# Optimization experiments

Hardware: AMD Instinct MI355X
Metric: run time of the kernel (lower is better)

## Reference

```python
import jax, jax.numpy as jnp
import numpy as np

N = 50000      # nodes per graph type
E = 600000     # directed edges
F = 64         # raw node feature length
H = 128        # hidden / embedding size (embedding == h, so no padding needed)
STEPS = 4
G = 64         # graphs in batch


def setup_inputs() -> dict:
    key = jax.random.key(0)
    ks = jax.random.split(key, 16)
    s = 1.0 / np.sqrt(H)
    inp = {
        "atom_x": jax.random.normal(ks[0], (N, F), jnp.float32),
        "voro_x": jax.random.normal(ks[1], (N, F), jnp.float32),
        "atom_edge_index": jax.random.randint(ks[2], (2, E), 0, N, jnp.int64),
        "voro_edge_index": jax.random.randint(ks[3], (2, E), 0, N, jnp.int64),
        "batch": jnp.sort(jax.random.randint(ks[4], (N,), 0, G, jnp.int64)),
        # input embeddings (bias=False)
        "W_atom_in": jax.random.normal(ks[5], (F, H), jnp.float32) / np.sqrt(F),
        "W_voro_in": jax.random.normal(ks[6], (F, H), jnp.float32) / np.sqrt(F),
        # GatedGraphConv per-step message weights [STEPS, H, H]
        "atom_W": jax.random.normal(ks[7], (STEPS, H, H), jnp.float32) * s,
        "voro_W": jax.random.normal(ks[8], (STEPS, H, H), jnp.float32) * s,
        # GRUCell params (torch layout: W_ih [3H, H], gates ordered r, z, n)
        "atom_Wih": jax.random.normal(ks[9], (3 * H, H), jnp.float32) * s,
        "atom_Whh": jax.random.normal(ks[10], (3 * H, H), jnp.float32) * s,
        "atom_bih": jnp.zeros((3 * H,), jnp.float32),
        "atom_bhh": jnp.zeros((3 * H,), jnp.float32),
        "voro_Wih": jax.random.normal(ks[11], (3 * H, H), jnp.float32) * s,
        "voro_Whh": jax.random.normal(ks[12], (3 * H, H), jnp.float32) * s,
        "voro_bih": jnp.zeros((3 * H,), jnp.float32),
        "voro_bhh": jnp.zeros((3 * H,), jnp.float32),
        # prediction head Linear(2H, 1)
        "pred_W": jax.random.normal(ks[13], (2 * H, 1), jnp.float32) * s,
        "pred_b": jnp.zeros((1,), jnp.float32),
    }
    return inp


def _gated_graph_conv(x, edge_index, W, Wih, Whh, bih, bhh):
    """PyG GatedGraphConv with aggr='add': per step, m = h @ W_l, scatter-add
    messages from source to target, then GRUCell(m, h)."""
    src, dst = edge_index[0], edge_index[1]

    def step(h, Wl):
        m = h @ Wl                                           # [N, H]
        agg = jax.ops.segment_sum(m[src], dst, num_segments=N)  # gather+scatter-add
        gi = agg @ Wih.T + bih                               # input gates
        gh = h @ Whh.T + bhh                                 # hidden gates
        ir, iz, inn = jnp.split(gi, 3, axis=-1)
        hr, hz, hn = jnp.split(gh, 3, axis=-1)
        r = jax.nn.sigmoid(ir + hr)
        z = jax.nn.sigmoid(iz + hz)
        n = jnp.tanh(inn + r * hn)
        h_new = (1.0 - z) * n + z * h
        return h_new, None

    h, _ = jax.lax.scan(step, x, W)
    return h


def _mean_pool(x, batch):
    s = jax.ops.segment_sum(x, batch, num_segments=G)
    cnt = jax.ops.segment_sum(jnp.ones((x.shape[0],), x.dtype), batch, num_segments=G)
    return s / jnp.maximum(cnt, 1.0)[:, None]


def reference(atom_x, voro_x, atom_edge_index, voro_edge_index, batch,
              W_atom_in, W_voro_in, atom_W, voro_W,
              atom_Wih, atom_Whh, atom_bih, atom_bhh,
              voro_Wih, voro_Whh, voro_bih, voro_bhh,
              pred_W, pred_b):
    a = jnp.tanh(atom_x @ W_atom_in)                         # [N, H]
    v = jnp.tanh(voro_x @ W_voro_in)                         # [N, H]
    a = _gated_graph_conv(a, atom_edge_index, atom_W, atom_Wih, atom_Whh, atom_bih, atom_bhh)
    v = _gated_graph_conv(v, voro_edge_index, voro_W, voro_Wih, voro_Whh, voro_bih, voro_bhh)
    a = jax.nn.relu(_mean_pool(a, batch))                    # [G, H]
    v = jax.nn.relu(_mean_pool(v, batch))                    # [G, H]
    g = jnp.concatenate([a, v], axis=1)                      # [G, 2H]
    return (g @ pred_W + pred_b)[:, 0]                       # [G]
```

## Files before the change

kernel.cpp:

```cpp
#include <hip/hip_runtime.h>
#include <hip/hip_fp16.h>
#include <math.h>

#define HDIM 128
typedef unsigned short u16;
typedef __attribute__((ext_vector_type(8))) short bf16x8;
typedef __attribute__((ext_vector_type(4))) float f32x4;

__device__ __forceinline__ u16 f2bf(float x) {
    unsigned u = __float_as_uint(x);
    u = (u + 0x7FFFu + ((u >> 16) & 1u)) >> 16;
    return (u16)u;
}
__device__ __forceinline__ float bf2f(u16 h) {
    return __uint_as_float(((unsigned)h) << 16);
}
__device__ __forceinline__ bf16x8 ld8(const u16* p) {
    return *reinterpret_cast<const bf16x8*>(p);
}
__device__ __forceinline__ void split8(const float* v, bf16x8& hi, bf16x8& lo) {
#pragma unroll
    for (int j = 0; j < 8; ++j) {
        unsigned u = __float_as_uint(v[j]);
        unsigned h = (u + 0x7FFFu + ((u >> 16) & 1u)) >> 16;
        float rem = v[j] - __uint_as_float(h << 16);
        hi[j] = (short)h;
        lo[j] = (short)(__float_as_uint(rem) >> 16);
    }
}
__device__ __forceinline__ float2 up2(unsigned u) {
    __half2 h = *reinterpret_cast<__half2*>(&u);
    float2 f; f.x = __low2float(h); f.y = __high2float(h); return f;
}
__device__ __forceinline__ u16 f2h(float x) {
    __half t = __float2half(x);
    return *reinterpret_cast<u16*>(&t);
}
#define MFMA(acc, a, b) acc = __builtin_amdgcn_mfma_f32_16x16x32_bf16(a, b, acc, 0, 0, 0)

__global__ __launch_bounds__(256) void prep_wfull(const float* __restrict__ Ws,
                                                  const float* __restrict__ Wih,
                                                  u16* __restrict__ hi, u16* __restrict__ lo) {
    int s = blockIdx.y;
    int idx = blockIdx.x * 256 + threadIdx.x;
    int c2 = idx >> 7, r = idx & 127;
    const float* wr = Ws + (size_t)s * 16384 + (size_t)r * 128;
    const float* wc = Wih + (size_t)c2 * 128;
    float acc = 0.f;
#pragma unroll 8
    for (int k = 0; k < 128; k += 4) {
        float4 a = *reinterpret_cast<const float4*>(wr + k);
        float4 b = *reinterpret_cast<const float4*>(wc + k);
        acc += a.x * b.x + a.y * b.y + a.z * b.z + a.w * b.w;
    }
    size_t o = (size_t)s * 49152 + idx;
    u16 h = f2bf(acc);
    hi[o] = h; lo[o] = f2bf(acc - bf2f(h));
}

__global__ __launch_bounds__(256) void prep_split(const float* __restrict__ W,
                                                  u16* __restrict__ hi, u16* __restrict__ lo, int n) {
    int i = blockIdx.x * 256 + threadIdx.x;
    if (i < n) { float v = W[i]; u16 h = f2bf(v); hi[i] = h; lo[i] = f2bf(v - bf2f(h)); }
}

__global__ __launch_bounds__(256) void prep_win(const float* __restrict__ W,
                                                u16* __restrict__ hi, u16* __restrict__ lo) {
    int idx = blockIdx.x * 256 + threadIdx.x;
    int r = idx >> 6, c = idx & 63;
    float v = W[(size_t)c * 128 + r];
    u16 h = f2bf(v);
    hi[idx] = h; lo[idx] = f2bf(v - bf2f(h));
}

__global__ __launch_bounds__(256) void split_x2(const float* __restrict__ x0, const float* __restrict__ x1,
                                                u16* __restrict__ hi0, u16* __restrict__ lo0,
                                                u16* __restrict__ hi1, u16* __restrict__ lo1,
                                                int n, int ntot) {
    int i = blockIdx.x * 256 + threadIdx.x;
    if (i >= ntot) return;
    const float* x = blockIdx.y ? x1 : x0;
    u16* hi = blockIdx.y ? hi1 : hi0;
    u16* lo = blockIdx.y ? lo1 : lo0;
    float v = (i < n) ? x[i] : 0.f;
    u16 h = f2bf(v);
    hi[i] = h; lo[i] = f2bf(v - bf2f(h));
}

__global__ __launch_bounds__(256) void embed_k(const u16* __restrict__ Xhi0, const u16* __restrict__ Xlo0,
                                               const u16* __restrict__ Xhi1, const u16* __restrict__ Xlo1,
                                               const u16* __restrict__ Bhi0, const u16* __restrict__ Blo0,
                                               const u16* __restrict__ Bhi1, const u16* __restrict__ Blo1,
                                               float* __restrict__ Hf0, float* __restrict__ Hf1,
                                               u16* __restrict__ Hh0, u16* __restrict__ Hh1) {
    const int by = blockIdx.y;
    const u16* Xhi = by ? Xhi1 : Xhi0;  const u16* Xlo = by ? Xlo1 : Xlo0;
    const u16* Bhi = by ? Bhi1 : Bhi0;  const u16* Blo = by ? Blo1 : Blo0;
    float* Hf = by ? Hf1 : Hf0;
    u16* Hh = by ? Hh1 : Hh0;
    const int tid = threadIdx.x, wave = tid >> 6, lane = tid & 63;
    const int row0 = blockIdx.x * 32, cs = wave * 32;
    const int lr = lane & 15, lk = (lane >> 4) * 8;
    f32x4 acc[2][2];
#pragma unroll
    for (int i = 0; i < 2; ++i)
#pragma unroll
        for (int j = 0; j < 2; ++j) acc[i][j] = (f32x4)0.f;
#pragma unroll
    for (int kc = 0; kc < 2; ++kc) {
        const size_t ao = (size_t)(row0 + lr) * 64 + kc * 32 + lk;
        bf16x8 ah0 = ld8(Xhi + ao), ah1 = ld8(Xhi + ao + 16 * 64);
        bf16x8 al0 = ld8(Xlo + ao), al1 = ld8(Xlo + ao + 16 * 64);
#pragma unroll
        for (int cf = 0; cf < 2; ++cf) {
            const size_t bo = (size_t)(cs + cf * 16 + lr) * 64 + kc * 32 + lk;
            bf16x8 bh = ld8(Bhi + bo), bl = ld8(Blo + bo);
            MFMA(acc[0][cf], ah0, bh); MFMA(acc[0][cf], ah0, bl); MFMA(acc[0][cf], al0, bh);
            MFMA(acc[1][cf], ah1, bh); MFMA(acc[1][cf], ah1, bl); MFMA(acc[1][cf], al1, bh);
        }
    }
#pragma unroll
    for (int rf = 0; rf < 2; ++rf)
#pragma unroll
        for (int cf = 0; cf < 2; ++cf)
#pragma unroll
            for (int rg = 0; rg < 4; ++rg) {
                int row = row0 + rf * 16 + (lane >> 4) * 4 + rg;
                int col = cs + cf * 16 + lr;
                float v = tanhf(acc[rf][cf][rg]);
                size_t o = (size_t)row * HDIM + col;
                Hf[o] = v;
                Hh[o] = f2h(v);
            }
}

__global__ __launch_bounds__(512, 4) void step_k(const float* __restrict__ Hf0, const float* __restrict__ Hf1,
                                                 const u16* __restrict__ Hh0, const u16* __restrict__ Hh1,
                                                 const int* __restrict__ ro0, const int* __restrict__ ro1,
                                                 const int* __restrict__ ss0, const int* __restrict__ ss1,
                                                 const u16* __restrict__ Wf0h, const u16* __restrict__ Wf0l,
                                                 const u16* __restrict__ Wf1h, const u16* __restrict__ Wf1l,
                                                 const u16* __restrict__ Wh0h, const u16* __restrict__ Wh0l,
                                                 const u16* __restrict__ Wh1h, const u16* __restrict__ Wh1l,
                                                 const float* __restrict__ bi0, const float* __restrict__ bh0,
                                                 const float* __restrict__ bi1, const float* __restrict__ bh1,
                                                 float* __restrict__ Hn0, float* __restrict__ Hn1,
                                                 u16* __restrict__ Hnh0, u16* __restrict__ Hnh1, int Nn) {
    __shared__ u16 agh[32][136];
    __shared__ u16 agl[32][136];
    __shared__ u16 hhh[32][136];
    __shared__ u16 hhl[32][136];
    __shared__ int eidx[1024];
    const int by = blockIdx.y;
    const float* Hf = by ? Hf1 : Hf0;
    const u16* Hh = by ? Hh1 : Hh0;
    const int* row_off = by ? ro1 : ro0;
    const int* ssrc = by ? ss1 : ss0;
    const int tid = threadIdx.x, wave = tid >> 6, lane = tid & 63;
    const int row0 = blockIdx.x * 32;

    const int rowEnd = (row0 + 32 < Nn) ? row0 + 32 : Nn;
    const int eLo = row_off[row0];
    const int nE = row_off[rowEnd] - eLo;
    for (int i = tid; i < nE && i < 1024; i += 512) eidx[i] = ssrc[eLo + i];
    __syncthreads();

#pragma unroll
    for (int q = 0; q < 4; ++q) {
        const int nl = wave * 4 + q;
        const int node = row0 + nl;
        float ax = 0.f, ay = 0.f;
        if (node < Nn) {
            int lo = row_off[node] - eLo, hi = row_off[node + 1] - eLo;
            int hiS = (hi < 1024) ? hi : 1024;
            int i = lo;
            for (; i + 12 <= hiS; i += 12) {
                unsigned u[12];
#pragma unroll
                for (int j = 0; j < 12; ++j)
                    u[j] = *reinterpret_cast<const unsigned*>(Hh + (size_t)eidx[i + j] * HDIM + lane * 2);
#pragma unroll
                for (int j = 0; j < 12; ++j) { float2 v = up2(u[j]); ax += v.x; ay += v.y; }
            }
            for (; i + 4 <= hiS; i += 4) {
                unsigned u[4];
#pragma unroll
                for (int j = 0; j < 4; ++j)
                    u[j] = *reinterpret_cast<const unsigned*>(Hh + (size_t)eidx[i + j] * HDIM + lane * 2);
#pragma unroll
                for (int j = 0; j < 4; ++j) { float2 v = up2(u[j]); ax += v.x; ay += v.y; }
            }
            for (; i < hiS; ++i) {
                float2 v = up2(*reinterpret_cast<const unsigned*>(Hh + (size_t)eidx[i] * HDIM + lane * 2));
                ax += v.x; ay += v.y;
            }
            for (; i < hi; ++i) {
                float2 v = up2(*reinterpret_cast<const unsigned*>(Hh + (size_t)ssrc[eLo + i] * HDIM + lane * 2));
                ax += v.x; ay += v.y;
            }
        }
        u16 hx = f2bf(ax), hy = f2bf(ay);
        u16 lx = f2bf(ax - bf2f(hx)), ly = f2bf(ay - bf2f(hy));
        *reinterpret_cast<unsigned*>(&agh[nl][lane * 2]) = (unsigned)hx | ((unsigned)hy << 16);
        *reinterpret_cast<unsigned*>(&agl[nl][lane * 2]) = (unsigned)lx | ((unsigned)ly << 16);
    }

    {
        const int r = tid >> 4, c0 = (tid & 15) * 8;
        float v[8];
        const float* hp = Hf + (size_t)(row0 + r) * HDIM + c0;
        *reinterpret_cast<float4*>(&v[0]) = *reinterpret_cast<const float4*>(hp);
        *reinterpret_cast<float4*>(&v[4]) = *reinterpret_cast<const float4*>(hp + 4);
        bf16x8 hi, lo;
        split8(v, hi, lo);
        *reinterpret_cast<bf16x8*>(&hhh[r][c0]) = hi;
        *reinterpret_cast<bf16x8*>(&hhl[r][c0]) = lo;
    }
    __syncthreads();

    const u16* Wfhi = by ? Wf1h : Wf0h;  const u16* Wflo = by ? Wf1l : Wf0l;
    const u16* Whhi = by ? Wh1h : Wh0h;  const u16* Whlo = by ? Wh1l : Wh0l;
    const float* bih = by ? bi1 : bi0;   const float* bhh = by ? bh1 : bh0;
    float* Hnf = by ? Hn1 : Hn0;
    u16* Hnh = by ? Hnh1 : Hnh0;
    const int lr = lane & 15, lk = (lane >> 4) * 8, cs = wave * 16;
    f32x4 accI[2][3], accH[2][3];
#pragma unroll
    for (int rf = 0; rf < 2; ++rf)
#pragma unroll
        for (int g = 0; g < 3; ++g) { accI[rf][g] = (f32x4)0.f; accH[rf][g] = (f32x4)0.f; }
#pragma unroll
    for (int kc = 0; kc < 4; ++kc) {
        bf16x8 ga[2], gl[2], ha[2], hl[2];
#pragma unroll
        for (int rf = 0; rf < 2; ++rf) {
            const int rr = rf * 16 + lr, cc = kc * 32 + lk;
            ga[rf] = *reinterpret_cast<const bf16x8*>(&agh[rr][cc]);
            gl[rf] = *reinterpret_cast<const bf16x8*>(&agl[rr][cc]);
            ha[rf] = *reinterpret_cast<const bf16x8*>(&hhh[rr][cc]);
            hl[rf] = *reinterpret_cast<const bf16x8*>(&hhl[rr][cc]);
        }
#pragma unroll
        for (int g = 0; g < 3; ++g) {
            const size_t bo = (size_t)(g * 128 + cs + lr) * HDIM + kc * 32 + lk;
            bf16x8 fh = ld8(Wfhi + bo), fl = ld8(Wflo + bo);
            bf16x8 wh = ld8(Whhi + bo), wl = ld8(Whlo + bo);
#pragma unroll
            for (int rf = 0; rf < 2; ++rf) {
                MFMA(accI[rf][g], ga[rf], fh); MFMA(accI[rf][g], ga[rf], fl); MFMA(accI[rf][g], gl[rf], fh);
                MFMA(accH[rf][g], ha[rf], wh); MFMA(accH[rf][g], ha[rf], wl); MFMA(accH[rf][g], hl[rf], wh);
            }
        }
    }
    const int c = cs + lr;
    const float bir = bih[c], biz = bih[128 + c], bin = bih[256 + c];
    const float bhr = bhh[c], bhz = bhh[128 + c], bhn = bhh[256 + c];
#pragma unroll
    for (int rf = 0; rf < 2; ++rf)
#pragma unroll
        for (int rg = 0; rg < 4; ++rg) {
            const int rl = rf * 16 + (lane >> 4) * 4 + rg;
            const int row = row0 + rl;
            float gir = accI[rf][0][rg] + bir;
            float giz = accI[rf][1][rg] + biz;
            float gin = accI[rf][2][rg] + bin;
            float ghr = accH[rf][0][rg] + bhr;
            float ghz = accH[rf][1][rg] + bhz;
            float ghn = accH[rf][2][rg] + bhn;
            float r = 1.f / (1.f + expf(-(gir + ghr)));
            float z = 1.f / (1.f + expf(-(giz + ghz)));
            float nn = tanhf(gin + r * ghn);
            float hold = bf2f(hhh[rl][c]) + bf2f(hhl[rl][c]);
            float hn = (1.f - z) * nn + z * hold;
            size_t o = (size_t)row * HDIM + c;
            Hnf[o] = hn;
            Hnh[o] = f2h(hn);
        }
}

__global__ void zero_int2(int* p0, int* p1, int n) {
    int i = blockIdx.x * 256 + threadIdx.x;
    int* p = blockIdx.y ? p1 : p0;
    if (i < n) p[i] = 0;
}

__global__ void hist_k2(const int* __restrict__ d0, const int* __restrict__ d1,
                        int* __restrict__ c0, int* __restrict__ c1, int E) {
    int e = blockIdx.x * 256 + threadIdx.x;
    const int* dst = blockIdx.y ? d1 : d0;
    int* cnt = blockIdx.y ? c1 : c0;
    if (e < E) atomicAdd(&cnt[dst[e]], 1);
}

__global__ __launch_bounds__(1024) void scan_k2(int* __restrict__ c0, int* __restrict__ r0,
                                                int* __restrict__ c1, int* __restrict__ r1, int n) {
    int* cnt_cursor = blockIdx.x ? c1 : c0;
    int* row_off = blockIdx.x ? r1 : r0;
    __shared__ int wsum[16];
    __shared__ int carry_s;
    const int tid = threadIdx.x, lane = tid & 63, wv = tid >> 6;
    if (tid == 0) carry_s = 0;
    __syncthreads();
    for (int base = 0; base < n; base += 1024) {
        int i = base + tid;
        int v = (i < n) ? cnt_cursor[i] : 0;
        int x = v;
#pragma unroll
        for (int off = 1; off < 64; off <<= 1) {
            int t = __shfl_up(x, off);
            if (lane >= off) x += t;
        }
        if (lane == 63) wsum[wv] = x;
        __syncthreads();
        if (wv == 0 && lane < 16) {
            int s = wsum[lane];
#pragma unroll
            for (int off = 1; off < 16; off <<= 1) {
                int t = __shfl_up(s, off);
                if (lane >= off) s += t;
            }
            wsum[lane] = s;
        }
        __syncthreads();
        int wbase = (wv == 0) ? 0 : wsum[wv - 1];
        int carry = carry_s;
        int total = wsum[15];
        int excl = carry + wbase + x - v;
        if (i < n) { row_off[i] = excl; cnt_cursor[i] = excl; }
        __syncthreads();
        if (tid == 0) carry_s = carry + total;
        __syncthreads();
    }
    if (tid == 0) row_off[n] = carry_s;
}

__global__ void scatter_k2(const int* __restrict__ s0, const int* __restrict__ d0,
                           const int* __restrict__ s1, const int* __restrict__ d1,
                           int* __restrict__ c0, int* __restrict__ c1,
                           int* __restrict__ o0, int* __restrict__ o1, int E) {
    int e = blockIdx.x * 256 + threadIdx.x;
    const int* src = blockIdx.y ? s1 : s0;
    const int* dst = blockIdx.y ? d1 : d0;
    int* cursor = blockIdx.y ? c1 : c0;
    int* ssrc = blockIdx.y ? o1 : o0;
    if (e < E) {
        int p = atomicAdd(&cursor[dst[e]], 1);
        ssrc[p] = src[e];
    }
}

__global__ __launch_bounds__(256) void pool_k(const float* __restrict__ H0, const float* __restrict__ H1,
                                              const int* __restrict__ batch,
                                              float* __restrict__ p0, float* __restrict__ p1, int M) {
    const float* Hf = blockIdx.y ? H1 : H0;
    float* pooled = blockIdx.y ? p1 : p0;
    __shared__ int lo_s, hi_s;
    __shared__ float smx[256], smy[256];
    int g = blockIdx.x;
    if (threadIdx.x == 0) {
        int lo = 0, hi = M;
        while (lo < hi) { int mid = (lo + hi) >> 1; if (batch[mid] < g) lo = mid + 1; else hi = mid; }
        lo_s = lo;
        int lo2 = lo, hi2 = M;
        while (lo2 < hi2) { int mid = (lo2 + hi2) >> 1; if (batch[mid] < g + 1) lo2 = mid + 1; else hi2 = mid; }
        hi_s = lo2;
    }
    __syncthreads();
    int lo = lo_s, hi = hi_s;
    int c2 = threadIdx.x & 63, quarter = threadIdx.x >> 6;
    float ax = 0.f, ay = 0.f;
    for (int i = lo + quarter; i < hi; i += 4) {
        float2 v = *reinterpret_cast<const float2*>(Hf + (size_t)i * HDIM + c2 * 2);
        ax += v.x; ay += v.y;
    }
    smx[threadIdx.x] = ax; smy[threadIdx.x] = ay;
    __syncthreads();
    if (quarter == 0) {
        float sx = smx[c2] + smx[c2 + 64] + smx[c2 + 128] + smx[c2 + 192];
        float sy = smy[c2] + smy[c2 + 64] + smy[c2 + 128] + smy[c2 + 192];
        float cnt = (float)(hi - lo); if (cnt < 1.f) cnt = 1.f;
        pooled[g * HDIM + c2 * 2]     = fmaxf(sx / cnt, 0.f);
        pooled[g * HDIM + c2 * 2 + 1] = fmaxf(sy / cnt, 0.f);
    }
}

__global__ void pred_kernel(const float* __restrict__ pa, const float* __restrict__ pv,
                            const float* __restrict__ pW, const float* __restrict__ pb,
                            float* __restrict__ out) {
    int g = blockIdx.x, lane = threadIdx.x;
    float s = pa[g * HDIM + lane] * pW[lane]
            + pa[g * HDIM + 64 + lane] * pW[64 + lane]
            + pv[g * HDIM + lane] * pW[HDIM + lane]
            + pv[g * HDIM + 64 + lane] * pW[192 + lane];
    for (int off = 32; off; off >>= 1) s += __shfl_down(s, off);
    if (lane == 0) out[g] = s + pb[0];
}

extern "C" void kernel_launch(void* const* d_in, const int* in_sizes, int n_in,
                              void* d_out, int out_size, void* d_ws, size_t ws_size,
                              hipStream_t stream) {
    const float* atom_x   = (const float*)d_in[0];
    const float* voro_x   = (const float*)d_in[1];
    const int*   atom_ei  = (const int*)d_in[2];
    const int*   voro_ei  = (const int*)d_in[3];
    const int*   batch    = (const int*)d_in[4];
    const float* W_at_in  = (const float*)d_in[5];
    const float* W_vo_in  = (const float*)d_in[6];
    const float* atom_W   = (const float*)d_in[7];
    const float* voro_W   = (const float*)d_in[8];
    const float* atom_Wih = (const float*)d_in[9];
    const float* atom_Whh = (const float*)d_in[10];
    const float* atom_bih = (const float*)d_in[11];
    const float* atom_bhh = (const float*)d_in[12];
    const float* voro_Wih = (const float*)d_in[13];
    const float* voro_Whh = (const float*)d_in[14];
    const float* voro_bih = (const float*)d_in[15];
    const float* voro_bhh = (const float*)d_in[16];
    const float* pred_W   = (const float*)d_in[17];
    const float* pred_b   = (const float*)d_in[18];
    float* out = (float*)d_out;

    const int Nn = in_sizes[4];
    const int Ee = in_sizes[2] / 2;
    const int Gg = out_size;
    const int Npad = (Nn + 31) & ~31;

    char* base = (char*)d_ws;
    size_t off = 0;
    auto alloc = [&](size_t bytes) -> char* {
        char* p = base + off;
        off = (off + bytes + 255) & ~(size_t)255;
        return p;
    };

    float *Hf[2], *Hnf[2];
    u16 *HhA[2], *HhB[2];
    u16 *Xhi[2], *Xlo[2];
    u16 *WfHi[2], *WfLo[2], *WhHi[2], *WhLo[2], *WnHi[2], *WnLo[2];
    int *row_off[2], *cursor[2], *ssrc[2];
    for (int t = 0; t < 2; ++t) {
        Hf[t]  = (float*)alloc((size_t)Npad * HDIM * 4);
        Hnf[t] = (float*)alloc((size_t)Npad * HDIM * 4);
        HhA[t] = (u16*)alloc((size_t)Npad * HDIM * 2);
        HhB[t] = (u16*)alloc((size_t)Npad * HDIM * 2);
        Xhi[t] = (u16*)Hnf[t];
        Xlo[t] = Xhi[t] + (size_t)Npad * 64;
        WfHi[t] = (u16*)alloc(4 * 49152 * 2); WfLo[t] = (u16*)alloc(4 * 49152 * 2);
        WhHi[t] = (u16*)alloc(384 * 128 * 2); WhLo[t] = (u16*)alloc(384 * 128 * 2);
        WnHi[t] = (u16*)alloc(128 * 64 * 2);  WnLo[t] = (u16*)alloc(128 * 64 * 2);
        row_off[t] = (int*)alloc((size_t)(Nn + 1) * 4);
        cursor[t]  = (int*)alloc((size_t)Nn * 4);
        ssrc[t]    = (int*)alloc((size_t)Ee * 4);
    }
    float* pooledA = (float*)alloc((size_t)Gg * HDIM * 4);
    float* pooledV = (float*)alloc((size_t)Gg * HDIM * 4);

    const float* Wst[2] = {atom_W, voro_W};
    const float* Wih[2] = {atom_Wih, voro_Wih};
    const float* Whh[2] = {atom_Whh, voro_Whh};
    const float* Win[2] = {W_at_in, W_vo_in};

    for (int t = 0; t < 2; ++t) {
        prep_wfull<<<dim3(192, 4), 256, 0, stream>>>(Wst[t], Wih[t], WfHi[t], WfLo[t]);
        prep_split<<<192, 256, 0, stream>>>(Whh[t], WhHi[t], WhLo[t], 384 * 128);
        prep_win<<<32, 256, 0, stream>>>(Win[t], WnHi[t], WnLo[t]);
    }

    const int eb  = (Ee + 255) / 256;
    const int nb  = (Nn + 255) / 256;
    const int gbs = Npad / 32;

    split_x2<<<dim3((Npad * 64 + 255) / 256, 2), 256, 0, stream>>>(
        atom_x, voro_x, Xhi[0], Xlo[0], Xhi[1], Xlo[1], Nn * 64, Npad * 64);
    embed_k<<<dim3(gbs, 2), 256, 0, stream>>>(Xhi[0], Xlo[0], Xhi[1], Xlo[1],
                                              WnHi[0], WnLo[0], WnHi[1], WnLo[1],
                                              Hf[0], Hf[1], HhA[0], HhA[1]);

    zero_int2<<<dim3(nb, 2), 256, 0, stream>>>(cursor[0], cursor[1], Nn);
    hist_k2<<<dim3(eb, 2), 256, 0, stream>>>(atom_ei + Ee, voro_ei + Ee, cursor[0], cursor[1], Ee);
    scan_k2<<<2, 1024, 0, stream>>>(cursor[0], row_off[0], cursor[1], row_off[1], Nn);
    scatter_k2<<<dim3(eb, 2), 256, 0, stream>>>(atom_ei, atom_ei + Ee, voro_ei, voro_ei + Ee,
                                                cursor[0], cursor[1], ssrc[0], ssrc[1], Ee);

    float *hA0 = Hf[0], *hB0 = Hnf[0], *hA1 = Hf[1], *hB1 = Hnf[1];
    u16 *gA0 = HhA[0], *gB0 = HhB[0], *gA1 = HhA[1], *gB1 = HhB[1];
    for (int s = 0; s < 4; ++s) {
        step_k<<<dim3(gbs, 2), 512, 0, stream>>>(
            hA0, hA1, gA0, gA1, row_off[0], row_off[1], ssrc[0], ssrc[1],
            WfHi[0] + (size_t)s * 49152, WfLo[0] + (size_t)s * 49152,
            WfHi[1] + (size_t)s * 49152, WfLo[1] + (size_t)s * 49152,
            WhHi[0], WhLo[0], WhHi[1], WhLo[1],
            atom_bih, atom_bhh, voro_bih, voro_bhh,
            hB0, hB1, gB0, gB1, Nn);
        float* tp;
        tp = hA0; hA0 = hB0; hB0 = tp;
        tp = hA1; hA1 = hB1; hB1 = tp;
        u16* up;
        up = gA0; gA0 = gB0; gB0 = up;
        up = gA1; gA1 = gB1; gB1 = up;
    }
    pool_k<<<dim3(Gg, 2), 256, 0, stream>>>(hA0, hA1, batch, pooledA, pooledV, Nn);
    pred_kernel<<<Gg, 64, 0, stream>>>(pooledA, pooledV, pred_W, pred_b, out);
}
```

Baseline: 1.166 ms.

## Warp-specialize GRU step into persistent gather/MFMA pipeline with fp16-only state

The step kernel becomes persistent: 256 blocks per graph type each loop over a range of 32-row tiles. Four waves gather neighbor sums and the old state into a double-buffered LDS tile while eight waves run the GRU matmuls on the previous tile. The input and hidden weights are concatenated into a single K=256 matrix, so one MFMA loop covers both. The fp32 hidden-state copy is dropped and only fp16 state is kept, which removes the fp32 reads and writes but makes the recurrent state carry fp16 rounding between steps.

```diff
diff --git a/kernel.cpp b/kernel.cpp
--- a/kernel.cpp
+++ b/kernel.cpp
@@ -18,16 +18,6 @@
 __device__ __forceinline__ bf16x8 ld8(const u16* p) {
     return *reinterpret_cast<const bf16x8*>(p);
 }
-__device__ __forceinline__ void split8(const float* v, bf16x8& hi, bf16x8& lo) {
-#pragma unroll
-    for (int j = 0; j < 8; ++j) {
-        unsigned u = __float_as_uint(v[j]);
-        unsigned h = (u + 0x7FFFu + ((u >> 16) & 1u)) >> 16;
-        float rem = v[j] - __uint_as_float(h << 16);
-        hi[j] = (short)h;
-        lo[j] = (short)(__float_as_uint(rem) >> 16);
-    }
-}
 __device__ __forceinline__ float2 up2(unsigned u) {
     __half2 h = *reinterpret_cast<__half2*>(&u);
     float2 f; f.x = __low2float(h); f.y = __high2float(h); return f;
@@ -38,30 +28,31 @@
 }
 #define MFMA(acc, a, b) acc = __builtin_amdgcn_mfma_f32_16x16x32_bf16(a, b, acc, 0, 0, 0)
 
-__global__ __launch_bounds__(256) void prep_wfull(const float* __restrict__ Ws,
-                                                  const float* __restrict__ Wih,
-                                                  u16* __restrict__ hi, u16* __restrict__ lo) {
+__global__ __launch_bounds__(256) void prep_wcat(const float* __restrict__ Ws,
+                                                 const float* __restrict__ Wih,
+                                                 const float* __restrict__ Whh,
+                                                 u16* __restrict__ hi, u16* __restrict__ lo) {
     int s = blockIdx.y;
     int idx = blockIdx.x * 256 + threadIdx.x;
-    int c2 = idx >> 7, r = idx & 127;
-    const float* wr = Ws + (size_t)s * 16384 + (size_t)r * 128;
-    const float* wc = Wih + (size_t)c2 * 128;
-    float acc = 0.f;
+    int c = idx >> 8, k = idx & 255;
+    float v;
+    if (k < 128) {
+        const float* wr = Ws + (size_t)s * 16384 + (size_t)k * 128;
+        const float* wc = Wih + (size_t)c * 128;
+        float acc = 0.f;
 #pragma unroll 8
-    for (int k = 0; k < 128; k += 4) {
-        float4 a = *reinterpret_cast<const float4*>(wr + k);
-        float4 b = *reinterpret_cast<const float4*>(wc + k);
-        acc += a.x * b.x + a.y * b.y + a.z * b.z + a.w * b.w;
-    }
-    size_t o = (size_t)s * 49152 + idx;
-    u16 h = f2bf(acc);
-    hi[o] = h; lo[o] = f2bf(acc - bf2f(h));
-}
-
-__global__ __launch_bounds__(256) void prep_split(const float* __restrict__ W,
-                                                  u16* __restrict__ hi, u16* __restrict__ lo, int n) {
-    int i = blockIdx.x * 256 + threadIdx.x;
-    if (i < n) { float v = W[i]; u16 h = f2bf(v); hi[i] = h; lo[i] = f2bf(v - bf2f(h)); }
+        for (int m = 0; m < 128; m += 4) {
+            float4 a = *reinterpret_cast<const float4*>(wr + m);
+            float4 b = *reinterpret_cast<const float4*>(wc + m);
+            acc += a.x * b.x + a.y * b.y + a.z * b.z + a.w * b.w;
+        }
+        v = acc;
+    } else {
+        v = Whh[(size_t)c * 128 + (k - 128)];
+    }
+    size_t o = (size_t)s * 98304 + idx;
+    u16 h = f2bf(v);
+    hi[o] = h; lo[o] = f2bf(v - bf2f(h));
 }
 
 __global__ __launch_bounds__(256) void prep_win(const float* __restrict__ W,
@@ -91,12 +82,10 @@
                                                const u16* __restrict__ Xhi1, const u16* __restrict__ Xlo1,
                                                const u16* __restrict__ Bhi0, const u16* __restrict__ Blo0,
                                                const u16* __restrict__ Bhi1, const u16* __restrict__ Blo1,
-                                               float* __restrict__ Hf0, float* __restrict__ Hf1,
                                                u16* __restrict__ Hh0, u16* __restrict__ Hh1) {
     const int by = blockIdx.y;
     const u16* Xhi = by ? Xhi1 : Xhi0;  const u16* Xlo = by ? Xlo1 : Xlo0;
     const u16* Bhi = by ? Bhi1 : Bhi0;  const u16* Blo = by ? Blo1 : Blo0;
-    float* Hf = by ? Hf1 : Hf0;
     u16* Hh = by ? Hh1 : Hh0;
     const int tid = threadIdx.x, wave = tid >> 6, lane = tid & 63;
     const int row0 = blockIdx.x * 32, cs = wave * 32;
@@ -127,155 +116,136 @@
             for (int rg = 0; rg < 4; ++rg) {
                 int row = row0 + rf * 16 + (lane >> 4) * 4 + rg;
                 int col = cs + cf * 16 + lr;
-                float v = tanhf(acc[rf][cf][rg]);
-                size_t o = (size_t)row * HDIM + col;
-                Hf[o] = v;
-                Hh[o] = f2h(v);
+                Hh[(size_t)row * HDIM + col] = f2h(tanhf(acc[rf][cf][rg]));
             }
 }
 
-__global__ __launch_bounds__(512, 4) void step_k(const float* __restrict__ Hf0, const float* __restrict__ Hf1,
-                                                 const u16* __restrict__ Hh0, const u16* __restrict__ Hh1,
+__global__ __launch_bounds__(768, 6) void step_k(const u16* __restrict__ Hh0, const u16* __restrict__ Hh1,
                                                  const int* __restrict__ ro0, const int* __restrict__ ro1,
                                                  const int* __restrict__ ss0, const int* __restrict__ ss1,
-                                                 const u16* __restrict__ Wf0h, const u16* __restrict__ Wf0l,
-                                                 const u16* __restrict__ Wf1h, const u16* __restrict__ Wf1l,
-                                                 const u16* __restrict__ Wh0h, const u16* __restrict__ Wh0l,
-                                                 const u16* __restrict__ Wh1h, const u16* __restrict__ Wh1l,
+                                                 const u16* __restrict__ Wc0h, const u16* __restrict__ Wc0l,
+                                                 const u16* __restrict__ Wc1h, const u16* __restrict__ Wc1l,
                                                  const float* __restrict__ bi0, const float* __restrict__ bh0,
                                                  const float* __restrict__ bi1, const float* __restrict__ bh1,
-                                                 float* __restrict__ Hn0, float* __restrict__ Hn1,
-                                                 u16* __restrict__ Hnh0, u16* __restrict__ Hnh1, int Nn) {
-    __shared__ u16 agh[32][136];
-    __shared__ u16 agl[32][136];
-    __shared__ u16 hhh[32][136];
-    __shared__ u16 hhl[32][136];
-    __shared__ int eidx[1024];
+                                                 u16* __restrict__ Hn0, u16* __restrict__ Hn1,
+                                                 int Nn, int nTiles, int nBx) {
+    __shared__ u16 ash[2][32][264];
+    __shared__ u16 asl[2][32][264];
     const int by = blockIdx.y;
-    const float* Hf = by ? Hf1 : Hf0;
     const u16* Hh = by ? Hh1 : Hh0;
     const int* row_off = by ? ro1 : ro0;
     const int* ssrc = by ? ss1 : ss0;
+    const u16* Wch = by ? Wc1h : Wc0h;
+    const u16* Wcl = by ? Wc1l : Wc0l;
+    const float* bih = by ? bi1 : bi0;
+    const float* bhh = by ? bh1 : bh0;
+    u16* Hnh = by ? Hn1 : Hn0;
     const int tid = threadIdx.x, wave = tid >> 6, lane = tid & 63;
-    const int row0 = blockIdx.x * 32;
-
-    const int rowEnd = (row0 + 32 < Nn) ? row0 + 32 : Nn;
-    const int eLo = row_off[row0];
-    const int nE = row_off[rowEnd] - eLo;
-    for (int i = tid; i < nE && i < 1024; i += 512) eidx[i] = ssrc[eLo + i];
-    __syncthreads();
-
-#pragma unroll
-    for (int q = 0; q < 4; ++q) {
-        const int nl = wave * 4 + q;
-        const int node = row0 + nl;
-        float ax = 0.f, ay = 0.f;
-        if (node < Nn) {
-            int lo = row_off[node] - eLo, hi = row_off[node + 1] - eLo;
-            int hiS = (hi < 1024) ? hi : 1024;
-            int i = lo;
-            for (; i + 12 <= hiS; i += 12) {
-                unsigned u[12];
-#pragma unroll
-                for (int j = 0; j < 12; ++j)
-                    u[j] = *reinterpret_cast<const unsigned*>(Hh + (size_t)eidx[i + j] * HDIM + lane * 2);
-#pragma unroll
-                for (int j = 0; j < 12; ++j) { float2 v = up2(u[j]); ax += v.x; ay += v.y; }
+    const int lr = lane & 15, lk = (lane >> 4) * 8;
+    const int t0 = (int)(((long long)blockIdx.x * nTiles) / nBx);
+    const int t1 = (int)(((long long)(blockIdx.x + 1) * nTiles) / nBx);
+
+    const int cs = (wave - 4) * 16;
+    float bir = 0.f, biz = 0.f, bin_ = 0.f, bhr = 0.f, bhz = 0.f, bhn = 0.f;
+    if (wave >= 4) {
+        const int c = cs + lr;
+        bir = bih[c]; biz = bih[128 + c]; bin_ = bih[256 + c];
+        bhr = bhh[c]; bhz = bhh[128 + c]; bhn = bhh[256 + c];
+    }
+
+    for (int t = t0; t <= t1; ++t) {
+        if (wave < 4) {
+            if (t < t1) {
+                const int buf = t & 1;
+                const int row0 = t * 32;
+#pragma unroll 2
+                for (int q = 0; q < 8; ++q) {
+                    const int nl = (wave << 3) + q;
+                    const int node = row0 + nl;
+                    float ax = 0.f, ay = 0.f, hx = 0.f, hy = 0.f;
+                    if (node < Nn) {
+                        int elo = __builtin_amdgcn_readfirstlane(row_off[node]);
+                        int ehi = __builtin_amdgcn_readfirstlane(row_off[node + 1]);
+                        int i = elo;
+                        for (; i + 8 <= ehi; i += 8) {
+                            unsigned u[8];
+#pragma unroll
+                            for (int j = 0; j < 8; ++j) {
+                                const int idx = ssrc[i + j];
+                                u[j] = *reinterpret_cast<const unsigned*>(Hh + (size_t)idx * HDIM + lane * 2);
+                            }
+#pragma unroll
+                            for (int j = 0; j < 8; ++j) { float2 v = up2(u[j]); ax += v.x; ay += v.y; }
+                        }
+                        for (; i < ehi; ++i) {
+                            const int idx = ssrc[i];
+                            float2 v = up2(*reinterpret_cast<const unsigned*>(Hh + (size_t)idx * HDIM + lane * 2));
+                            ax += v.x; ay += v.y;
+                        }
+                        float2 hv = up2(*reinterpret_cast<const unsigned*>(Hh + (size_t)node * HDIM + lane * 2));
+                        hx = hv.x; hy = hv.y;
+                    }
+                    u16 ahx = f2bf(ax), ahy = f2bf(ay);
+                    u16 alx = f2bf(ax - bf2f(ahx)), aly = f2bf(ay - bf2f(ahy));
+                    *reinterpret_cast<unsigned*>(&ash[buf][nl][lane * 2]) = (unsigned)ahx | ((unsigned)ahy << 16);
+                    *reinterpret_cast<unsigned*>(&asl[buf][nl][lane * 2]) = (unsigned)alx | ((unsigned)aly << 16);
+                    u16 hhx = f2bf(hx), hhy = f2bf(hy);
+                    u16 hlx = f2bf(hx - bf2f(hhx)), hly = f2bf(hy - bf2f(hhy));
+                    *reinterpret_cast<unsigned*>(&ash[buf][nl][128 + lane * 2]) = (unsigned)hhx | ((unsigned)hhy << 16);
+                    *reinterpret_cast<unsigned*>(&asl[buf][nl][128 + lane * 2]) = (unsigned)hlx | ((unsigned)hly << 16);
+                }
             }
-            for (; i + 4 <= hiS; i += 4) {
-                unsigned u[4];
-#pragma unroll
-                for (int j = 0; j < 4; ++j)
-                    u[j] = *reinterpret_cast<const unsigned*>(Hh + (size_t)eidx[i + j] * HDIM + lane * 2);
-#pragma unroll
-                for (int j = 0; j < 4; ++j) { float2 v = up2(u[j]); ax += v.x; ay += v.y; }
+        } else if (t > t0) {
+            const int tt = t - 1;
+            const int buf = tt & 1;
+            const int row0 = tt * 32;
+            f32x4 arz[2][2], ain[2], ahn[2];
+#pragma unroll
+            for (int rf = 0; rf < 2; ++rf) {
+                arz[rf][0] = (f32x4)0.f; arz[rf][1] = (f32x4)0.f;
+                ain[rf] = (f32x4)0.f; ahn[rf] = (f32x4)0.f;
             }
-            for (; i < hiS; ++i) {
-                float2 v = up2(*reinterpret_cast<const unsigned*>(Hh + (size_t)eidx[i] * HDIM + lane * 2));
-                ax += v.x; ay += v.y;
+#pragma unroll
+            for (int kc = 0; kc < 8; ++kc) {
+                bf16x8 ah[2], al[2];
+#pragma unroll
+                for (int rf = 0; rf < 2; ++rf) {
+                    const int rr = rf * 16 + lr, cc = kc * 32 + lk;
+                    ah[rf] = *reinterpret_cast<const bf16x8*>(&ash[buf][rr][cc]);
+                    al[rf] = *reinterpret_cast<const bf16x8*>(&asl[buf][rr][cc]);
+                }
+#pragma unroll
+                for (int g = 0; g < 3; ++g) {
+                    const size_t bo = (size_t)(g * 128 + cs + lr) * 256 + kc * 32 + lk;
+                    bf16x8 bh = ld8(Wch + bo), bl = ld8(Wcl + bo);
+#pragma unroll
+                    for (int rf = 0; rf < 2; ++rf) {
+                        if (g < 2) {
+                            MFMA(arz[rf][g], ah[rf], bh); MFMA(arz[rf][g], ah[rf], bl); MFMA(arz[rf][g], al[rf], bh);
+                        } else if (kc < 4) {
+                            MFMA(ain[rf], ah[rf], bh); MFMA(ain[rf], ah[rf], bl); MFMA(ain[rf], al[rf], bh);
+                        } else {
+                            MFMA(ahn[rf], ah[rf], bh); MFMA(ahn[rf], ah[rf], bl); MFMA(ahn[rf], al[rf], bh);
+                        }
+                    }
+                }
             }
-            for (; i < hi; ++i) {
-                float2 v = up2(*reinterpret_cast<const unsigned*>(Hh + (size_t)ssrc[eLo + i] * HDIM + lane * 2));
-                ax += v.x; ay += v.y;
-            }
+            const int c = cs + lr;
+#pragma unroll
+            for (int rf = 0; rf < 2; ++rf)
+#pragma unroll
+                for (int rg = 0; rg < 4; ++rg) {
+                    const int rl = rf * 16 + (lane >> 4) * 4 + rg;
+                    float r = 1.f / (1.f + expf(-(arz[rf][0][rg] + bir + bhr)));
+                    float z = 1.f / (1.f + expf(-(arz[rf][1][rg] + biz + bhz)));
+                    float nn = tanhf(ain[rf][rg] + bin_ + r * (ahn[rf][rg] + bhn));
+                    float hold = bf2f(ash[buf][rl][128 + c]) + bf2f(asl[buf][rl][128 + c]);
+                    float hn = (1.f - z) * nn + z * hold;
+                    Hnh[(size_t)(row0 + rl) * HDIM + c] = f2h(hn);
+                }
         }
-        u16 hx = f2bf(ax), hy = f2bf(ay);
-        u16 lx = f2bf(ax - bf2f(hx)), ly = f2bf(ay - bf2f(hy));
-        *reinterpret_cast<unsigned*>(&agh[nl][lane * 2]) = (unsigned)hx | ((unsigned)hy << 16);
-        *reinterpret_cast<unsigned*>(&agl[nl][lane * 2]) = (unsigned)lx | ((unsigned)ly << 16);
-    }
-
-    {
-        const int r = tid >> 4, c0 = (tid & 15) * 8;
-        float v[8];
-        const float* hp = Hf + (size_t)(row0 + r) * HDIM + c0;
-        *reinterpret_cast<float4*>(&v[0]) = *reinterpret_cast<const float4*>(hp);
-        *reinterpret_cast<float4*>(&v[4]) = *reinterpret_cast<const float4*>(hp + 4);
-        bf16x8 hi, lo;
-        split8(v, hi, lo);
-        *reinterpret_cast<bf16x8*>(&hhh[r][c0]) = hi;
-        *reinterpret_cast<bf16x8*>(&hhl[r][c0]) = lo;
-    }
-    __syncthreads();
-
-    const u16* Wfhi = by ? Wf1h : Wf0h;  const u16* Wflo = by ? Wf1l : Wf0l;
-    const u16* Whhi = by ? Wh1h : Wh0h;  const u16* Whlo = by ? Wh1l : Wh0l;
-    const float* bih = by ? bi1 : bi0;   const float* bhh = by ? bh1 : bh0;
-    float* Hnf = by ? Hn1 : Hn0;
-    u16* Hnh = by ? Hnh1 : Hnh0;
-    const int lr = lane & 15, lk = (lane >> 4) * 8, cs = wave * 16;
-    f32x4 accI[2][3], accH[2][3];
-#pragma unroll
-    for (int rf = 0; rf < 2; ++rf)
-#pragma unroll
-        for (int g = 0; g < 3; ++g) { accI[rf][g] = (f32x4)0.f; accH[rf][g] = (f32x4)0.f; }
-#pragma unroll
-    for (int kc = 0; kc < 4; ++kc) {
-        bf16x8 ga[2], gl[2], ha[2], hl[2];
-#pragma unroll
-        for (int rf = 0; rf < 2; ++rf) {
-            const int rr = rf * 16 + lr, cc = kc * 32 + lk;
-            ga[rf] = *reinterpret_cast<const bf16x8*>(&agh[rr][cc]);
-            gl[rf] = *reinterpret_cast<const bf16x8*>(&agl[rr][cc]);
-            ha[rf] = *reinterpret_cast<const bf16x8*>(&hhh[rr][cc]);
-            hl[rf] = *reinterpret_cast<const bf16x8*>(&hhl[rr][cc]);
-        }
-#pragma unroll
-        for (int g = 0; g < 3; ++g) {
-            const size_t bo = (size_t)(g * 128 + cs + lr) * HDIM + kc * 32 + lk;
-            bf16x8 fh = ld8(Wfhi + bo), fl = ld8(Wflo + bo);
-            bf16x8 wh = ld8(Whhi + bo), wl = ld8(Whlo + bo);
-#pragma unroll
-            for (int rf = 0; rf < 2; ++rf) {
-                MFMA(accI[rf][g], ga[rf], fh); MFMA(accI[rf][g], ga[rf], fl); MFMA(accI[rf][g], gl[rf], fh);
-                MFMA(accH[rf][g], ha[rf], wh); MFMA(accH[rf][g], ha[rf], wl); MFMA(accH[rf][g], hl[rf], wh);
-            }
-        }
-    }
-    const int c = cs + lr;
-    const float bir = bih[c], biz = bih[128 + c], bin = bih[256 + c];
-    const float bhr = bhh[c], bhz = bhh[128 + c], bhn = bhh[256 + c];
-#pragma unroll
-    for (int rf = 0; rf < 2; ++rf)
-#pragma unroll
-        for (int rg = 0; rg < 4; ++rg) {
-            const int rl = rf * 16 + (lane >> 4) * 4 + rg;
-            const int row = row0 + rl;
-            float gir = accI[rf][0][rg] + bir;
-            float giz = accI[rf][1][rg] + biz;
-            float gin = accI[rf][2][rg] + bin;
-            float ghr = accH[rf][0][rg] + bhr;
-            float ghz = accH[rf][1][rg] + bhz;
-            float ghn = accH[rf][2][rg] + bhn;
-            float r = 1.f / (1.f + expf(-(gir + ghr)));
-            float z = 1.f / (1.f + expf(-(giz + ghz)));
-            float nn = tanhf(gin + r * ghn);
-            float hold = bf2f(hhh[rl][c]) + bf2f(hhl[rl][c]);
-            float hn = (1.f - z) * nn + z * hold;
-            size_t o = (size_t)row * HDIM + c;
-            Hnf[o] = hn;
-            Hnh[o] = f2h(hn);
-        }
+        __syncthreads();
+    }
 }
 
 __global__ void zero_int2(int* p0, int* p1, int n) {
@@ -349,10 +319,10 @@
     }
 }
 
-__global__ __launch_bounds__(256) void pool_k(const float* __restrict__ H0, const float* __restrict__ H1,
+__global__ __launch_bounds__(256) void pool_k(const u16* __restrict__ H0, const u16* __restrict__ H1,
                                               const int* __restrict__ batch,
                                               float* __restrict__ p0, float* __restrict__ p1, int M) {
-    const float* Hf = blockIdx.y ? H1 : H0;
+    const u16* Hf = blockIdx.y ? H1 : H0;
     float* pooled = blockIdx.y ? p1 : p0;
     __shared__ int lo_s, hi_s;
     __shared__ float smx[256], smy[256];
@@ -370,7 +340,7 @@
     int c2 = threadIdx.x & 63, quarter = threadIdx.x >> 6;
     float ax = 0.f, ay = 0.f;
     for (int i = lo + quarter; i < hi; i += 4) {
-        float2 v = *reinterpret_cast<const float2*>(Hf + (size_t)i * HDIM + c2 * 2);
+        float2 v = up2(*reinterpret_cast<const unsigned*>(Hf + (size_t)i * HDIM + c2 * 2));
         ax += v.x; ay += v.y;
     }
     smx[threadIdx.x] = ax; smy[threadIdx.x] = ay;
@@ -424,6 +394,8 @@
     const int Ee = in_sizes[2] / 2;
     const int Gg = out_size;
     const int Npad = (Nn + 31) & ~31;
+    const int nTiles = Npad / 32;
+    const int nBx = 256;
 
     char* base = (char*)d_ws;
     size_t off = 0;
@@ -433,21 +405,19 @@
         return p;
     };
 
-    float *Hf[2], *Hnf[2];
     u16 *HhA[2], *HhB[2];
     u16 *Xhi[2], *Xlo[2];
-    u16 *WfHi[2], *WfLo[2], *WhHi[2], *WhLo[2], *WnHi[2], *WnLo[2];
+    u16 *WcH[2], *WcL[2], *WnHi[2], *WnLo[2];
     int *row_off[2], *cursor[2], *ssrc[2];
     for (int t = 0; t < 2; ++t) {
-        Hf[t]  = (float*)alloc((size_t)Npad * HDIM * 4);
-        Hnf[t] = (float*)alloc((size_t)Npad * HDIM * 4);
         HhA[t] = (u16*)alloc((size_t)Npad * HDIM * 2);
         HhB[t] = (u16*)alloc((size_t)Npad * HDIM * 2);
-        Xhi[t] = (u16*)Hnf[t];
-        Xlo[t] = Xhi[t] + (size_t)Npad * 64;
-        WfHi[t] = (u16*)alloc(4 * 49152 * 2); WfLo[t] = (u16*)alloc(4 * 49152 * 2);
-        WhHi[t] = (u16*)alloc(384 * 128 * 2); WhLo[t] = (u16*)alloc(384 * 128 * 2);
-        WnHi[t] = (u16*)alloc(128 * 64 * 2);  WnLo[t] = (u16*)alloc(128 * 64 * 2);
+        Xhi[t] = HhB[t];
+        Xlo[t] = HhB[t] + (size_t)Npad * 64;
+        WcH[t] = (u16*)alloc((size_t)4 * 98304 * 2);
+        WcL[t] = (u16*)alloc((size_t)4 * 98304 * 2);
+        WnHi[t] = (u16*)alloc(128 * 64 * 2);
+        WnLo[t] = (u16*)alloc(128 * 64 * 2);
         row_off[t] = (int*)alloc((size_t)(Nn + 1) * 4);
         cursor[t]  = (int*)alloc((size_t)Nn * 4);
         ssrc[t]    = (int*)alloc((size_t)Ee * 4);
@@ -461,20 +431,19 @@
     const float* Win[2] = {W_at_in, W_vo_in};
 
     for (int t = 0; t < 2; ++t) {
-        prep_wfull<<<dim3(192, 4), 256, 0, stream>>>(Wst[t], Wih[t], WfHi[t], WfLo[t]);
-        prep_split<<<192, 256, 0, stream>>>(Whh[t], WhHi[t], WhLo[t], 384 * 128);
+        prep_wcat<<<dim3(384, 4), 256, 0, stream>>>(Wst[t], Wih[t], Whh[t], WcH[t], WcL[t]);
         prep_win<<<32, 256, 0, stream>>>(Win[t], WnHi[t], WnLo[t]);
     }
 
     const int eb  = (Ee + 255) / 256;
     const int nb  = (Nn + 255) / 256;
-    const int gbs = Npad / 32;
+    const int gbe = Npad / 32;
 
     split_x2<<<dim3((Npad * 64 + 255) / 256, 2), 256, 0, stream>>>(
         atom_x, voro_x, Xhi[0], Xlo[0], Xhi[1], Xlo[1], Nn * 64, Npad * 64);
-    embed_k<<<dim3(gbs, 2), 256, 0, stream>>>(Xhi[0], Xlo[0], Xhi[1], Xlo[1],
+    embed_k<<<dim3(gbe, 2), 256, 0, stream>>>(Xhi[0], Xlo[0], Xhi[1], Xlo[1],
                                               WnHi[0], WnLo[0], WnHi[1], WnLo[1],
-                                              Hf[0], Hf[1], HhA[0], HhA[1]);
+                                              HhA[0], HhA[1]);
 
     zero_int2<<<dim3(nb, 2), 256, 0, stream>>>(cursor[0], cursor[1], Nn);
     hist_k2<<<dim3(eb, 2), 256, 0, stream>>>(atom_ei + Ee, voro_ei + Ee, cursor[0], cursor[1], Ee);
@@ -482,23 +451,18 @@
     scatter_k2<<<dim3(eb, 2), 256, 0, stream>>>(atom_ei, atom_ei + Ee, voro_ei, voro_ei + Ee,
                                                 cursor[0], cursor[1], ssrc[0], ssrc[1], Ee);
 
-    float *hA0 = Hf[0], *hB0 = Hnf[0], *hA1 = Hf[1], *hB1 = Hnf[1];
     u16 *gA0 = HhA[0], *gB0 = HhB[0], *gA1 = HhA[1], *gB1 = HhB[1];
     for (int s = 0; s < 4; ++s) {
-        step_k<<<dim3(gbs, 2), 512, 0, stream>>>(
-            hA0, hA1, gA0, gA1, row_off[0], row_off[1], ssrc[0], ssrc[1],
-            WfHi[0] + (size_t)s * 49152, WfLo[0] + (size_t)s * 49152,
-            WfHi[1] + (size_t)s * 49152, WfLo[1] + (size_t)s * 49152,
-            WhHi[0], WhLo[0], WhHi[1], WhLo[1],
+        step_k<<<dim3(nBx, 2), 768, 0, stream>>>(
+            gA0, gA1, row_off[0], row_off[1], ssrc[0], ssrc[1],
+            WcH[0] + (size_t)s * 98304, WcL[0] + (size_t)s * 98304,
+            WcH[1] + (size_t)s * 98304, WcL[1] + (size_t)s * 98304,
             atom_bih, atom_bhh, voro_bih, voro_bhh,
-            hB0, hB1, gB0, gB1, Nn);
-        float* tp;
-        tp = hA0; hA0 = hB0; hB0 = tp;
-        tp = hA1; hA1 = hB1; hB1 = tp;
+            gB0, gB1, Nn, nTiles, nBx);
         u16* up;
         up = gA0; gA0 = gB0; gB0 = up;
         up = gA1; gA1 = gB1; gB1 = up;
     }
-    pool_k<<<dim3(Gg, 2), 256, 0, stream>>>(hA0, hA1, batch, pooledA, pooledV, Nn);
+    pool_k<<<dim3(Gg, 2), 256, 0, stream>>>(gA0, gA1, batch, pooledA, pooledV, Nn);
     pred_kernel<<<Gg, 64, 0, stream>>>(pooledA, pooledV, pred_W, pred_b, out);
 }
```

Result: slower. 1.312 ms (+12.6%).
